# Performance work log

Measured on AMD Instinct MI355X. Metric: run time of the kernel, lower is better.

Reference implementation:

```python
import jax, jax.numpy as jnp
import numpy as np

B, S, HID, NH, AH, F = 1024, 100, 128, 2, 64, 2
DH = HID // NH          # item/pos head size = 64
DA = AH // NH           # attribute head size = 32
EPS = 1e-12


def setup_inputs() -> dict:
    key = jax.random.key(0)
    ks = iter(jax.random.split(key, 32))
    n = lambda shape, s=0.02: jax.random.normal(next(ks), shape, dtype=jnp.float32) * s
    inp = {
        "input_tensor": jax.random.normal(next(ks), (B, S, HID), dtype=jnp.float32),
        "attribute_table": jax.random.normal(next(ks), (F, B, S, AH), dtype=jnp.float32),
        "position_embedding": jax.random.normal(next(ks), (B, S, HID), dtype=jnp.float32),
        "attention_mask": jnp.zeros((B, 1, S, S), dtype=jnp.float32),
        # item / positional projections (stored [in, out])
        "Wq": n((HID, HID)), "bq": jnp.zeros((HID,), jnp.float32),
        "Wk": n((HID, HID)), "bk": jnp.zeros((HID,), jnp.float32),
        "Wv": n((HID, HID)), "bv": jnp.zeros((HID,), jnp.float32),
        "Wqp": n((HID, HID)), "bqp": jnp.zeros((HID,), jnp.float32),
        "Wkp": n((HID, HID)), "bkp": jnp.zeros((HID,), jnp.float32),
        # per-attribute projections, stacked over feat axis
        "Wq_attr": n((F, AH, AH)), "bq_attr": jnp.zeros((F, AH), jnp.float32),
        "Wk_attr": n((F, AH, AH)), "bk_attr": jnp.zeros((F, AH), jnp.float32),
        # gate fusion (VanillaAttentionX): Linear(S,S) -> ReLU -> Linear(S,1)
        "fuse_W1": n((S, S)), "fuse_b1": jnp.zeros((S,), jnp.float32),
        "fuse_W2": n((S, 1)), "fuse_b2": jnp.zeros((1,), jnp.float32),
        # output dense + LayerNorm
        "Wd": n((HID, HID)), "bd": jnp.zeros((HID,), jnp.float32),
        "ln_g": jnp.ones((HID,), jnp.float32), "ln_b": jnp.zeros((HID,), jnp.float32),
    }
    return inp


def _split_heads(x, nh):  # [B,S,nh*d] -> [B,nh,S,d]
    b, s, hd = x.shape
    return x.reshape(b, s, nh, hd // nh).transpose(0, 2, 1, 3)


def reference(input_tensor, attribute_table, position_embedding, attention_mask,
              Wq, bq, Wk, bk, Wv, bv, Wqp, bqp, Wkp, bkp,
              Wq_attr, bq_attr, Wk_attr, bk_attr,
              fuse_W1, fuse_b1, fuse_W2, fuse_b2,
              Wd, bd, ln_g, ln_b):
    b, s, hid = input_tensor.shape
    # item / positional QKV
    q = _split_heads(input_tensor @ Wq + bq, NH)
    k = _split_heads(input_tensor @ Wk + bk, NH)
    v = _split_heads(input_tensor @ Wv + bv, NH)
    qp = _split_heads(position_embedding @ Wqp + bqp, NH)
    kp = _split_heads(position_embedding @ Wkp + bkp, NH)
    item_scores = jnp.einsum('bhqd,bhkd->bhqk', q, k)
    pos_scores = jnp.einsum('bhqd,bhkd->bhqk', qp, kp)
    # attribute score streams: [F,B,S,AH] -> [F,B,NH,S,DA]
    aq = jnp.einsum('fbsa,fao->fbso', attribute_table, Wq_attr) + bq_attr[:, None, None, :]
    ak = jnp.einsum('fbsa,fao->fbso', attribute_table, Wk_attr) + bk_attr[:, None, None, :]
    aq = aq.reshape(F, b, s, NH, DA).transpose(0, 1, 3, 2, 4)
    ak = ak.reshape(F, b, s, NH, DA).transpose(0, 1, 3, 2, 4)
    attr_scores = jnp.einsum('fbhqd,fbhkd->fbhqk', aq, ak)  # [F,B,NH,S,S]
    # gate fusion: stack streams on axis -2 -> [B,NH,S,F+2,S]
    stacked = jnp.concatenate([
        jnp.moveaxis(attr_scores, 0, 3),
        item_scores[:, :, :, None, :],
        pos_scores[:, :, :, None, :],
    ], axis=-2)
    energy = jax.nn.relu(stacked @ fuse_W1 + fuse_b1) @ fuse_W2 + fuse_b2  # [B,NH,S,F+2,1]
    gate_w = jax.nn.softmax(energy[..., 0], axis=-1)                       # [B,NH,S,F+2]
    fused = jnp.einsum('bhsfk,bhsf->bhsk', stacked, gate_w)                # [B,NH,S,S]
    scores = fused / jnp.sqrt(jnp.asarray(DH, fused.dtype)) + attention_mask
    probs = jax.nn.softmax(scores, axis=-1)
    ctx = jnp.einsum('bhqk,bhkd->bhqd', probs, v)
    ctx = ctx.transpose(0, 2, 1, 3).reshape(b, s, hid)
    h = ctx @ Wd + bd + input_tensor
    mu = jnp.mean(h, axis=-1, keepdims=True)
    var = jnp.mean((h - mu) ** 2, axis=-1, keepdims=True)
    return (h - mu) / jnp.sqrt(var + EPS) * ln_g + ln_b
```

## Files before the change

### kernel.cpp

```cpp
#include <hip/hip_runtime.h>
#include <hip/hip_bf16.h>

using bf16 = __hip_bfloat16;
using u16 = unsigned short;
typedef __attribute__((ext_vector_type(8))) short bf16x8;
typedef __attribute__((ext_vector_type(16))) float f32x16;

namespace {

constexpr int B_  = 1024;
constexpr int Sd  = 100;
constexpr int BS_ = B_ * Sd;

constexpr int NTHR = 1024;
constexpr int NW   = 16;

constexpr int STP = 420;
constexpr int STS = 104;
constexpr int QKP = 196;
constexpr int AP  = 132;
constexpr int ATP = 68;
constexpr int VTP = 116;
constexpr int W1P = 116;

constexpr int O_ST  = 0;
constexpr int O_SA0 = 0;
constexpr int O_SA1 = 26400;
constexpr int O_AT0 = 52800;
constexpr int O_AT1 = 66400;
constexpr int O_Q   = 84000;
constexpr int O_K   = 123200;
constexpr int O_VT  = 123200;
constexpr int O_E2S = 139200;
constexpr int LBYTES = 162400;

constexpr int WQT_E  = 0;
constexpr int WKT_E  = 16384;
constexpr int WQPT_E = 32768;
constexpr int WKPT_E = 49152;
constexpr int WVT_E  = 65536;
constexpr int WAT_E  = 81920;
constexpr int W1T_E  = 98304;
constexpr int WDT_E  = 112640;
constexpr int W1PG   = 112;
constexpr size_t WS_NEED = 129024ull * 2;

__device__ __forceinline__ float bfr(u16 u) {
  unsigned int x = ((unsigned int)u) << 16;
  float f; __builtin_memcpy(&f, &x, 4); return f;
}
__device__ __forceinline__ u16 f2bu(float x) {
  bf16 h = __float2bfloat16(x);
  u16 u; __builtin_memcpy(&u, &h, 2); return u;
}
__device__ __forceinline__ float4 ld4(const float* p) {
  return *reinterpret_cast<const float4*>(p);
}
__device__ __forceinline__ float wsum(float v) {
#pragma unroll
  for (int m = 32; m > 0; m >>= 1) v += __shfl_xor(v, m);
  return v;
}
__device__ __forceinline__ float wmax(float v) {
#pragma unroll
  for (int m = 32; m > 0; m >>= 1) v = fmaxf(v, __shfl_xor(v, m));
  return v;
}
__device__ __forceinline__ f32x16 zf16() {
  f32x16 z;
#pragma unroll
  for (int i = 0; i < 16; ++i) z[i] = 0.f;
  return z;
}
__device__ __forceinline__ f32x16 MFMA32(bf16x8 a, bf16x8 b, f32x16 c) {
  return __builtin_amdgcn_mfma_f32_32x32x16_bf16(a, b, c, 0, 0, 0);
}

__device__ __forceinline__ bf16x8 ld8(const u16* p) {
  const ushort4 a = *reinterpret_cast<const ushort4*>(p);
  const ushort4 b = *reinterpret_cast<const ushort4*>(p + 4);
  bf16x8 f;
  f[0] = (short)a.x; f[1] = (short)a.y; f[2] = (short)a.z; f[3] = (short)a.w;
  f[4] = (short)b.x; f[5] = (short)b.y; f[6] = (short)b.z; f[7] = (short)b.w;
  return f;
}
__device__ __forceinline__ bf16x8 ld8a(const u16* p) {
  return *reinterpret_cast<const bf16x8*>(p);
}

template <int L4>
__device__ __forceinline__ void stage_rows4(const float* __restrict__ src, u16* dst,
                                            int nrow, int pitch, int tid, int nthr) {
  for (int i = tid; i < (nrow << L4); i += nthr) {
    const int rr = i >> L4, cc = (i & ((1 << L4) - 1)) << 2;
    const float4 v = *reinterpret_cast<const float4*>(src + ((size_t)rr << (L4 + 2)) + cc);
    ushort4 o;
    o.x = f2bu(v.x); o.y = f2bu(v.y); o.z = f2bu(v.z); o.w = f2bu(v.w);
    *reinterpret_cast<ushort4*>(dst + rr * pitch + cc) = o;
  }
}
template <int LC>
__device__ __forceinline__ void stage_wt(const float* __restrict__ W, int ldw, int coff,
                                         u16* dst, int kd, int pitch, int tid, int nthr) {
  constexpr int NC = 1 << LC;
  for (int idx = tid; idx < NC * kd; idx += nthr) {
    const int k = idx >> LC, c = idx & (NC - 1);
    dst[c * pitch + k] = f2bu(W[k * ldw + coff + c]);
  }
}
__device__ __forceinline__ void stage_wt6(const float* __restrict__ W, int coff,
                                          u16* dst, int tid, int nthr) {
  stage_wt<6>(W, 128, coff, dst, 128, AP, tid, nthr);
}

template <int KD, bool TR, bool GB>
__device__ __forceinline__ void tile32(const u16* A, int apitch, const u16* Wt, int wpitch,
                                       const float* __restrict__ bias, u16* dst, int dpitch,
                                       int dbase, int m0, int n0, int l) {
  const int cr = l & 31, g = l >> 5;
  int ar = m0 + cr; if (ar >= Sd) ar = Sd - 1;
  const u16* ap = A + ar * apitch + g * 8;
  const u16* bp = Wt + (n0 + cr) * wpitch + g * 8;
  f32x16 acc = zf16();
#pragma unroll
  for (int k0 = 0; k0 < KD; k0 += 16)
    acc = MFMA32(ld8(ap + k0), GB ? ld8a(bp + k0) : ld8(bp + k0), acc);
  const float bvv = bias[n0 + cr];
#pragma unroll
  for (int i = 0; i < 16; ++i) {
    const int row = m0 + (i & 3) + 8 * (i >> 2) + 4 * g;
    if (row < Sd) {
      if (TR) dst[(n0 + cr) * dpitch + dbase + row] = f2bu(acc[i] + bvv);
      else    dst[row * dpitch + dbase + n0 + cr]   = f2bu(acc[i] + bvv);
    }
  }
}

__global__ __launch_bounds__(256) void prep_weights(
    const float* __restrict__ Wq, const float* __restrict__ Wk,
    const float* __restrict__ Wqp, const float* __restrict__ Wkp,
    const float* __restrict__ Wv, const float* __restrict__ Wqa,
    const float* __restrict__ Wka, const float* __restrict__ W1,
    const float* __restrict__ Wd, u16* __restrict__ ws) {
  const int t = blockIdx.x * 256 + threadIdx.x;
  const int NT = gridDim.x * 256;
  const float* srcs[5] = {Wq, Wk, Wqp, Wkp, Wv};
#pragma unroll
  for (int wsel = 0; wsel < 5; ++wsel) {
    u16* dst = ws + wsel * 16384;
    const float* src = srcs[wsel];
    for (int i = t; i < 16384; i += NT) {
      const int h = i >> 13, c = (i >> 7) & 63, k = i & 127;
      dst[i] = f2bu(src[k * 128 + h * 64 + c]);
    }
  }
  for (int i = t; i < 16384; i += NT) {
    const int pr = i >> 12, h = (i >> 11) & 1, c = (i >> 6) & 31, k = i & 63;
    const float* src = (pr & 1) ? Wka : Wqa;
    ws[WAT_E + i] = f2bu(src[(pr >> 1) * 4096 + k * 64 + h * 32 + c]);
  }
  for (int i = t; i < 14336; i += NT) {
    const int c = i / W1PG, k = i - c * W1PG;
    ws[W1T_E + i] = (c < Sd && k < Sd) ? f2bu(W1[k * Sd + c]) : (u16)0;
  }
  for (int i = t; i < 16384; i += NT) {
    const int c = i >> 7, k = i & 127;
    ws[WDT_E + i] = f2bu(Wd[k * 128 + c]);
  }
}

__global__ __launch_bounds__(NTHR) void attn_mega_p(
    const float* __restrict__ input, const float* __restrict__ attrT,
    const float* __restrict__ posE, const float* __restrict__ mask,
    const float* __restrict__ bq, const float* __restrict__ bk,
    const float* __restrict__ bv, const float* __restrict__ bqp,
    const float* __restrict__ bkp, const float* __restrict__ bqa,
    const float* __restrict__ bka, const float* __restrict__ b1,
    const float* __restrict__ W2, const u16* __restrict__ wsw,
    float* __restrict__ ctx) {
  __shared__ __align__(16) char L[LBYTES];
  u16* const ST  = (u16*)(L + O_ST);
  u16* const SA0 = (u16*)(L + O_SA0);
  u16* const SA1 = (u16*)(L + O_SA1);
  u16* const AT0 = (u16*)(L + O_AT0);
  u16* const AT1 = (u16*)(L + O_AT1);
  u16* const QC  = (u16*)(L + O_Q);
  u16* const KC  = (u16*)(L + O_K);
  u16* const VA  = (u16*)(L + O_Q);
  u16* const VT  = (u16*)(L + O_VT);
  float* const e2s = (float*)(L + O_E2S);

  const int tid = threadIdx.x;
  const int bh = blockIdx.x;
  const int b = bh >> 1, h = bh & 1;
  const size_t row0 = (size_t)b * Sd;
  const int l = tid & 63, w = tid >> 6;
  const int cr = l & 31, g = l >> 5;

  stage_rows4<5>(input + row0 * 128, SA0, 100, AP, tid, NTHR);
  float4 r2[4];
#pragma unroll
  for (int s = 0; s < 4; ++s) {
    const int fi = tid + s * NTHR;
    if (fi < 3200) r2[s] = ld4(posE + row0 * 128 + fi * 4);
  }
  __syncthreads();

  float4 r3[4];
#pragma unroll
  for (int s = 0; s < 4; ++s) {
    const int fi = tid + s * NTHR;
    if (fi < 1600)      r3[s] = ld4(attrT + (size_t)b * 6400 + fi * 4);
    else if (fi < 3200) r3[s] = ld4(attrT + (size_t)(B_ + b) * 6400 + (fi - 1600) * 4);
  }
#pragma unroll
  for (int s = 0; s < 4; ++s) {
    const int fi = tid + s * NTHR;
    if (fi < 3200) {
      ushort4 o;
      o.x = f2bu(r2[s].x); o.y = f2bu(r2[s].y); o.z = f2bu(r2[s].z); o.w = f2bu(r2[s].w);
      *reinterpret_cast<ushort4*>(SA1 + (fi >> 5) * AP + ((fi & 31) << 2)) = o;
    }
  }
  {
    const int pr = w >> 3, mt = (w >> 1) & 3, nt = w & 1;
    const u16* wg = wsw + (pr ? WKT_E : WQT_E) + h * 8192;
    tile32<128, false, true>(SA0, AP, wg, 128, (pr ? bk : bq) + h * 64,
                             pr ? KC : QC, QKP, 0, mt * 32, nt * 32, l);
  }
  __syncthreads();

#pragma unroll
  for (int s = 0; s < 4; ++s) {
    const int fi = tid + s * NTHR;
    if (fi < 1600) {
      ushort4 o;
      o.x = f2bu(r3[s].x); o.y = f2bu(r3[s].y); o.z = f2bu(r3[s].z); o.w = f2bu(r3[s].w);
      *reinterpret_cast<ushort4*>(AT0 + (fi >> 4) * ATP + ((fi & 15) << 2)) = o;
    } else if (fi < 3200) {
      const int f3 = fi - 1600;
      ushort4 o;
      o.x = f2bu(r3[s].x); o.y = f2bu(r3[s].y); o.z = f2bu(r3[s].z); o.w = f2bu(r3[s].w);
      *reinterpret_cast<ushort4*>(AT1 + (f3 >> 4) * ATP + ((f3 & 15) << 2)) = o;
    }
  }
  {
    const int pr = w >> 3, mt = (w >> 1) & 3, nt = w & 1;
    const u16* wg = wsw + (pr ? WKPT_E : WQPT_E) + h * 8192;
    tile32<128, false, true>(SA1, AP, wg, 128, (pr ? bkp : bqp) + h * 64,
                             pr ? KC : QC, QKP, 64, mt * 32, nt * 32, l);
  }
  __syncthreads();

  {
    const int pr = w >> 2, mt = w & 3;
    const u16* Asrc = (pr < 2) ? AT0 : AT1;
    const u16* wg = wsw + WAT_E + pr * 4096 + h * 2048;
    const float* bs = (pr == 0) ? bqa + h * 32 : (pr == 1) ? bka + h * 32
                     : (pr == 2) ? bqa + 64 + h * 32 : bka + 64 + h * 32;
    tile32<64, false, true>(Asrc, ATP, wg, 64, bs, (pr & 1) ? KC : QC, QKP,
                            128 + (pr >> 1) * 32, mt * 32, 0, l);
  }
  __syncthreads();

  {
    ushort4 z; z.x = z.y = z.z = z.w = 0;
    for (int q = tid; q < Sd; q += NTHR)
      *reinterpret_cast<ushort4*>(ST + q * STP + 416) = z;
  }
  {
    const int mt = w >> 2, nt = w & 3;
    const int m0 = mt * 32, n0 = nt * 32;
    int ar = m0 + cr; if (ar >= Sd) ar = Sd - 1;
    int br = n0 + cr; if (br >= Sd) br = Sd - 1;
    const u16* ap = QC + ar * QKP + g * 8;
    const u16* bp = KC + br * QKP + g * 8;
    f32x16 ai = zf16(), po = zf16(), a0 = zf16(), a1 = zf16();
    ai = MFMA32(ld8(ap + 0),   ld8(bp + 0),   ai);
    ai = MFMA32(ld8(ap + 16),  ld8(bp + 16),  ai);
    ai = MFMA32(ld8(ap + 32),  ld8(bp + 32),  ai);
    ai = MFMA32(ld8(ap + 48),  ld8(bp + 48),  ai);
    po = MFMA32(ld8(ap + 64),  ld8(bp + 64),  po);
    po = MFMA32(ld8(ap + 80),  ld8(bp + 80),  po);
    po = MFMA32(ld8(ap + 96),  ld8(bp + 96),  po);
    po = MFMA32(ld8(ap + 112), ld8(bp + 112), po);
    a0 = MFMA32(ld8(ap + 128), ld8(bp + 128), a0);
    a0 = MFMA32(ld8(ap + 144), ld8(bp + 144), a0);
    a1 = MFMA32(ld8(ap + 160), ld8(bp + 160), a1);
    a1 = MFMA32(ld8(ap + 176), ld8(bp + 176), a1);
    const int col = n0 + cr;
    if (col < STS) {
#pragma unroll
      for (int i = 0; i < 16; ++i) {
        const int row = m0 + (i & 3) + 8 * (i >> 2) + 4 * g;
        if (row < Sd) {
          u16* sp = ST + row * STP + col;
          sp[0]       = f2bu(a0[i]);
          sp[STS]     = f2bu(a1[i]);
          sp[2 * STS] = f2bu(ai[i]);
          sp[3 * STS] = f2bu(po[i]);
        }
      }
    }
  }
  __syncthreads();

  stage_rows4<5>(input + row0 * 128, VA, 100, AP, tid, NTHR);
  {
    ushort4 z; z.x = z.y = z.z = z.w = 0;
    for (int i2 = tid; i2 < 64 * VTP / 4; i2 += NTHR)
      *reinterpret_cast<ushort4*>(VT + i2 * 4) = z;
  }
  __syncthreads();

  {
    float b1v[4], w2v[4];
#pragma unroll
    for (int nt = 0; nt < 4; ++nt) {
      const int c = nt * 32 + cr;
      b1v[nt] = (c < Sd) ? b1[c] : 0.f;
      w2v[nt] = (c < Sd) ? W2[c] : 0.f;
    }
    const u16* wg1 = wsw + W1T_E;
    for (int mt = w; mt < 13; mt += NW) {
      const int m0 = mt * 32;
      int gr = m0 + cr; if (gr > 399) gr = 399;
      const u16* ap = ST + (gr >> 2) * STP + (gr & 3) * STS + g * 8;
      f32x16 c0 = zf16(), c1 = zf16(), c2 = zf16(), c3 = zf16();
#pragma unroll
      for (int k0 = 0; k0 < 112; k0 += 16) {
        const bf16x8 af = ld8(ap + k0);
        c0 = MFMA32(af, ld8a(wg1 + (cr)      * W1PG + g * 8 + k0), c0);
        c1 = MFMA32(af, ld8a(wg1 + (32 + cr) * W1PG + g * 8 + k0), c1);
        c2 = MFMA32(af, ld8a(wg1 + (64 + cr) * W1PG + g * 8 + k0), c2);
        c3 = MFMA32(af, ld8a(wg1 + (96 + cr) * W1PG + g * 8 + k0), c3);
      }
#pragma unroll
      for (int i = 0; i < 16; ++i) {
        float v = fmaxf(c0[i] + b1v[0], 0.f) * w2v[0]
                + fmaxf(c1[i] + b1v[1], 0.f) * w2v[1]
                + fmaxf(c2[i] + b1v[2], 0.f) * w2v[2]
                + fmaxf(c3[i] + b1v[3], 0.f) * w2v[3];
#pragma unroll
        for (int mm = 1; mm < 32; mm <<= 1) v += __shfl_xor(v, mm);
        if (cr == 0) {
          const int go = m0 + (i & 3) + 8 * (i >> 2) + 4 * g;
          if (go < 400) e2s[go] = v;
        }
      }
    }
  }
  __syncthreads();

  if (w < 8) {
    for (int q = w; q < Sd; q += 8) {
      const float* ez = e2s + q * 4;
      float e0 = ez[0], e1 = ez[1], e2v = ez[2], e3 = ez[3];
      const float mg = fmaxf(fmaxf(e0, e1), fmaxf(e2v, e3));
      e0 = __expf(e0 - mg); e1 = __expf(e1 - mg);
      e2v = __expf(e2v - mg); e3 = __expf(e3 - mg);
      const float ginv = 1.0f / (e0 + e1 + e2v + e3);
      const float g0v = e0 * ginv, g1v = e1 * ginv, g2v = e2v * ginv, g3v = e3 * ginv;
      u16* const sp = ST + q * STP;
      const float* const mp = mask + (size_t)b * 10000 + q * 100;
      float x1 = g0v * bfr(sp[l]) + g1v * bfr(sp[STS + l]) +
                 g2v * bfr(sp[2 * STS + l]) + g3v * bfr(sp[3 * STS + l]);
      x1 = x1 * 0.125f + mp[l];
      const bool v2 = (l < 36);
      float x2 = -3e38f;
      if (v2) {
        const int k2 = 64 + l;
        x2 = g0v * bfr(sp[k2]) + g1v * bfr(sp[STS + k2]) +
             g2v * bfr(sp[2 * STS + k2]) + g3v * bfr(sp[3 * STS + k2]);
        x2 = x2 * 0.125f + mp[k2];
      }
      const float M = wmax(fmaxf(x1, x2));
      const float ea = __expf(x1 - M);
      const float eb = v2 ? __expf(x2 - M) : 0.f;
      const float inv = 1.0f / wsum(ea + eb);
      sp[l] = f2bu(ea * inv);
      if (v2) sp[64 + l] = f2bu(eb * inv);
    }
  } else {
    const int u = w - 8;
    const int mt = u >> 1, nt = u & 1;
    tile32<128, true, true>(VA, AP, wsw + WVT_E + h * 8192, 128, bv + h * 64,
                            VT, VTP, 0, mt * 32, nt * 32, l);
  }
  __syncthreads();

  if (w < 8) {
    const int mt = w >> 1, nt = w & 1;
    const int m0 = mt * 32, n0 = nt * 32;
    int ar = m0 + cr; if (ar >= Sd) ar = Sd - 1;
    const u16* ap = ST + ar * STP + g * 8;
    const u16* bp = VT + (n0 + cr) * VTP + g * 8;
    f32x16 acc = zf16();
#pragma unroll
    for (int k0 = 0; k0 < 112; k0 += 16)
      acc = MFMA32(ld8(ap + k0), ld8(bp + k0), acc);
#pragma unroll
    for (int i = 0; i < 16; ++i) {
      const int row = m0 + (i & 3) + 8 * (i >> 2) + 4 * g;
      if (row < Sd)
        ctx[(row0 + row) * 128 + h * 64 + n0 + cr] = acc[i];
    }
  }
}

__global__ __launch_bounds__(512, 4) void dense_ln_p(
    const float* __restrict__ ctxg, const float* __restrict__ bd,
    const float* __restrict__ resid, const float* __restrict__ lng,
    const float* __restrict__ lnb, const u16* __restrict__ wsw,
    float* __restrict__ out) {
  __shared__ __align__(16) char L[67584];
  u16* const Ab = (u16*)L;
  u16* const Hs = (u16*)(L + 33792);
  const int tid = threadIdx.x;
  const size_t row0 = (size_t)blockIdx.x * 128;
  const int l = tid & 63, w = tid >> 6, cr = l & 31, g = l >> 5;

  stage_rows4<5>(ctxg + row0 * 128, Ab, 128, AP, tid, 512);
  __syncthreads();

  for (int u = w; u < 16; u += 8) {
    const int m0 = (u >> 2) * 32, n0 = (u & 3) * 32;
    const u16* ap = Ab + (m0 + cr) * AP + g * 8;
    const u16* bp = wsw + WDT_E + (n0 + cr) * 128 + g * 8;
    f32x16 acc = zf16();
#pragma unroll
    for (int k0 = 0; k0 < 128; k0 += 16)
      acc = MFMA32(ld8(ap + k0), ld8a(bp + k0), acc);
#pragma unroll
    for (int i = 0; i < 16; ++i) {
      const int row = m0 + (i & 3) + 8 * (i >> 2) + 4 * g;
      Hs[row * AP + n0 + cr] = f2bu(acc[i]);
    }
  }
  __syncthreads();

  for (int rr = w; rr < 128; rr += 8) {
    const size_t grow = row0 + rr;
    const float h1 = bfr(Hs[rr * AP + l])      + bd[l]      + resid[grow * 128 + l];
    const float h2 = bfr(Hs[rr * AP + 64 + l]) + bd[64 + l] + resid[grow * 128 + 64 + l];
    const float mu = wsum(h1 + h2) * (1.0f / 128.0f);
    const float d1 = h1 - mu, d2 = h2 - mu;
    const float var = wsum(d1 * d1 + d2 * d2) * (1.0f / 128.0f);
    const float rs = rsqrtf(var + 1e-12f);
    out[grow * 128 + l]      = d1 * rs * lng[l]      + lnb[l];
    out[grow * 128 + 64 + l] = d2 * rs * lng[64 + l] + lnb[64 + l];
  }
}

__global__ __launch_bounds__(NTHR) void attn_mega_fb(
    const float* __restrict__ input, const float* __restrict__ attrT,
    const float* __restrict__ posE, const float* __restrict__ mask,
    const float* __restrict__ Wq, const float* __restrict__ bq,
    const float* __restrict__ Wk, const float* __restrict__ bk,
    const float* __restrict__ Wv, const float* __restrict__ bv,
    const float* __restrict__ Wqp, const float* __restrict__ bqp,
    const float* __restrict__ Wkp, const float* __restrict__ bkp,
    const float* __restrict__ Wqa, const float* __restrict__ bqa,
    const float* __restrict__ Wka, const float* __restrict__ bka,
    const float* __restrict__ W1, const float* __restrict__ b1,
    const float* __restrict__ W2, float* __restrict__ ctx) {
  __shared__ __align__(16) char L[LBYTES];
  u16* const ST = (u16*)(L + O_ST);
  u16* const QC = (u16*)(L + O_Q);
  u16* const KC = (u16*)(L + O_K);
  u16* const SA  = (u16*)(L + O_ST);
  u16* const SW1 = (u16*)(L + O_ST + 26400);
  u16* const SW2 = (u16*)(L + O_ST + 43296);
  u16* const AT0  = (u16*)(L + O_ST);
  u16* const AT1  = (u16*)(L + O_ST + 13600);
  u16* const WA0Q = (u16*)(L + O_ST + 27200);
  u16* const WA0K = (u16*)(L + O_ST + 31552);
  u16* const WA1Q = (u16*)(L + O_ST + 35904);
  u16* const WA1K = (u16*)(L + O_ST + 40256);
  u16* const W1T = (u16*)(L + O_K);
  float* const e2s = (float*)(L + O_K + 32000);
  u16* const VA  = (u16*)(L + O_Q);
  u16* const WVT = (u16*)(L + O_K);
  u16* const VT  = (u16*)(L + O_K + 16896);

  const int tid = threadIdx.x;
  const int bh = blockIdx.x;
  const int b = bh >> 1, h = bh & 1;
  const size_t row0 = (size_t)b * Sd;
  const int l = tid & 63, w = tid >> 6;
  const int cr = l & 31, g = l >> 5;

  stage_rows4<5>(input + row0 * 128, SA, 100, AP, tid, NTHR);
  stage_wt6(Wq, h * 64, SW1, tid, NTHR);
  stage_wt6(Wk, h * 64, SW2, tid, NTHR);
  float4 r2[8];
#pragma unroll
  for (int s = 0; s < 8; ++s) {
    const int fi = tid + s * NTHR;
    if (fi < 3200) r2[s] = ld4(posE + row0 * 128 + fi * 4);
    else if (fi < 5248) {
      const int f2 = fi - 3200, k = f2 >> 4, c0 = (f2 & 15) << 2;
      r2[s] = ld4(Wqp + k * 128 + h * 64 + c0);
    } else if (fi < 7296) {
      const int f2 = fi - 5248, k = f2 >> 4, c0 = (f2 & 15) << 2;
      r2[s] = ld4(Wkp + k * 128 + h * 64 + c0);
    }
  }
  __syncthreads();
  {
    const int pr = w >> 3, mt = (w >> 1) & 3, nt = w & 1;
    tile32<128, false, false>(SA, AP, pr ? SW2 : SW1, AP, (pr ? bk : bq) + h * 64,
                              pr ? KC : QC, QKP, 0, mt * 32, nt * 32, l);
  }
  __syncthreads();
#pragma unroll
  for (int s = 0; s < 8; ++s) {
    const int fi = tid + s * NTHR;
    if (fi < 3200) {
      ushort4 o;
      o.x = f2bu(r2[s].x); o.y = f2bu(r2[s].y); o.z = f2bu(r2[s].z); o.w = f2bu(r2[s].w);
      *reinterpret_cast<ushort4*>(SA + (fi >> 5) * AP + ((fi & 31) << 2)) = o;
    } else if (fi < 5248) {
      const int f2 = fi - 3200, k = f2 >> 4, c0 = (f2 & 15) << 2;
      SW1[c0 * AP + k] = f2bu(r2[s].x); SW1[(c0 + 1) * AP + k] = f2bu(r2[s].y);
      SW1[(c0 + 2) * AP + k] = f2bu(r2[s].z); SW1[(c0 + 3) * AP + k] = f2bu(r2[s].w);
    } else if (fi < 7296) {
      const int f2 = fi - 5248, k = f2 >> 4, c0 = (f2 & 15) << 2;
      SW2[c0 * AP + k] = f2bu(r2[s].x); SW2[(c0 + 1) * AP + k] = f2bu(r2[s].y);
      SW2[(c0 + 2) * AP + k] = f2bu(r2[s].z); SW2[(c0 + 3) * AP + k] = f2bu(r2[s].w);
    }
  }
  float4 r3[6];
#pragma unroll
  for (int s = 0; s < 6; ++s) {
    const int fi = tid + s * NTHR;
    if (fi < 1600) r3[s] = ld4(attrT + (size_t)b * 6400 + fi * 4);
    else if (fi < 3200) r3[s] = ld4(attrT + (size_t)(B_ + b) * 6400 + (fi - 1600) * 4);
    else if (fi < 5248) {
      const int f3 = fi - 3200, which = f3 >> 9, fj = f3 & 511;
      const int k = fj >> 3, c0 = (fj & 7) << 2;
      const float* src = (which == 0) ? Wqa : (which == 1) ? Wka
                       : (which == 2) ? (Wqa + 4096) : (Wka + 4096);
      r3[s] = ld4(src + k * 64 + h * 32 + c0);
    }
  }
  __syncthreads();
  {
    const int pr = w >> 3, mt = (w >> 1) & 3, nt = w & 1;
    tile32<128, false, false>(SA, AP, pr ? SW2 : SW1, AP, (pr ? bkp : bqp) + h * 64,
                              pr ? KC : QC, QKP, 64, mt * 32, nt * 32, l);
  }
  __syncthreads();
#pragma unroll
  for (int s = 0; s < 6; ++s) {
    const int fi = tid + s * NTHR;
    if (fi < 1600) {
      ushort4 o;
      o.x = f2bu(r3[s].x); o.y = f2bu(r3[s].y); o.z = f2bu(r3[s].z); o.w = f2bu(r3[s].w);
      *reinterpret_cast<ushort4*>(AT0 + (fi >> 4) * ATP + ((fi & 15) << 2)) = o;
    } else if (fi < 3200) {
      const int f3 = fi - 1600;
      ushort4 o;
      o.x = f2bu(r3[s].x); o.y = f2bu(r3[s].y); o.z = f2bu(r3[s].z); o.w = f2bu(r3[s].w);
      *reinterpret_cast<ushort4*>(AT1 + (f3 >> 4) * ATP + ((f3 & 15) << 2)) = o;
    } else if (fi < 5248) {
      const int f3 = fi - 3200, which = f3 >> 9, fj = f3 & 511;
      const int k = fj >> 3, c0 = (fj & 7) << 2;
      u16* dst = (which == 0) ? WA0Q : (which == 1) ? WA0K
               : (which == 2) ? WA1Q : WA1K;
      dst[c0 * ATP + k] = f2bu(r3[s].x); dst[(c0 + 1) * ATP + k] = f2bu(r3[s].y);
      dst[(c0 + 2) * ATP + k] = f2bu(r3[s].z); dst[(c0 + 3) * ATP + k] = f2bu(r3[s].w);
    }
  }
  float4 r5[3];
#pragma unroll
  for (int s = 0; s < 3; ++s) {
    const int fi = tid + s * NTHR;
    if (fi < 2500) r5[s] = ld4(W1 + fi * 4);
  }
  __syncthreads();
  {
    const int pr = w >> 2, mt = w & 3;
    const u16* Asrc = (pr < 2) ? AT0 : AT1;
    const u16* Wt = (pr == 0) ? WA0Q : (pr == 1) ? WA0K : (pr == 2) ? WA1Q : WA1K;
    const float* bs = (pr == 0) ? bqa + h * 32 : (pr == 1) ? bka + h * 32
                     : (pr == 2) ? bqa + 64 + h * 32 : bka + 64 + h * 32;
    tile32<64, false, false>(Asrc, ATP, Wt, ATP, bs, (pr & 1) ? KC : QC, QKP,
                             128 + (pr >> 1) * 32, mt * 32, 0, l);
  }
  __syncthreads();
  {
    ushort4 z; z.x = z.y = z.z = z.w = 0;
    for (int q = tid; q < Sd; q += NTHR)
      *reinterpret_cast<ushort4*>(ST + q * STP + 416) = z;
  }
  {
    const int mt = w >> 2, nt = w & 3;
    const int m0 = mt * 32, n0 = nt * 32;
    int ar = m0 + cr; if (ar >= Sd) ar = Sd - 1;
    int br = n0 + cr; if (br >= Sd) br = Sd - 1;
    const u16* ap = QC + ar * QKP + g * 8;
    const u16* bp = KC + br * QKP + g * 8;
    f32x16 ai = zf16(), po = zf16(), a0 = zf16(), a1 = zf16();
    ai = MFMA32(ld8(ap + 0),   ld8(bp + 0),   ai);
    ai = MFMA32(ld8(ap + 16),  ld8(bp + 16),  ai);
    ai = MFMA32(ld8(ap + 32),  ld8(bp + 32),  ai);
    ai = MFMA32(ld8(ap + 48),  ld8(bp + 48),  ai);
    po = MFMA32(ld8(ap + 64),  ld8(bp + 64),  po);
    po = MFMA32(ld8(ap + 80),  ld8(bp + 80),  po);
    po = MFMA32(ld8(ap + 96),  ld8(bp + 96),  po);
    po = MFMA32(ld8(ap + 112), ld8(bp + 112), po);
    a0 = MFMA32(ld8(ap + 128), ld8(bp + 128), a0);
    a0 = MFMA32(ld8(ap + 144), ld8(bp + 144), a0);
    a1 = MFMA32(ld8(ap + 160), ld8(bp + 160), a1);
    a1 = MFMA32(ld8(ap + 176), ld8(bp + 176), a1);
    const int col = n0 + cr;
    if (col < STS) {
#pragma unroll
      for (int i = 0; i < 16; ++i) {
        const int row = m0 + (i & 3) + 8 * (i >> 2) + 4 * g;
        if (row < Sd) {
          u16* sp = ST + row * STP + col;
          sp[0]       = f2bu(a0[i]);
          sp[STS]     = f2bu(a1[i]);
          sp[2 * STS] = f2bu(ai[i]);
          sp[3 * STS] = f2bu(po[i]);
        }
      }
    }
  }
  __syncthreads();
  {
    ushort4 z; z.x = z.y = z.z = z.w = 0;
    if (tid < 812)
      *reinterpret_cast<ushort4*>(W1T + 11600 + tid * 4) = z;
    if (tid < 400) {
      const int c = tid >> 2, kq = 100 + ((tid & 3) << 2);
      *reinterpret_cast<ushort4*>(W1T + c * W1P + kq) = z;
    }
  }
  if (tid < 8) ((u16*)(L + O_Q))[tid] = 0;
#pragma unroll
  for (int s = 0; s < 3; ++s) {
    const int fi = tid + s * NTHR;
    if (fi < 2500) {
#pragma unroll
      for (int j = 0; j < 4; ++j) {
        const int o = fi * 4 + j;
        const int k = o / 100, c = o - k * 100;
        W1T[c * W1P + k] = f2bu((j == 0) ? r5[s].x : (j == 1) ? r5[s].y
                                : (j == 2) ? r5[s].z : r5[s].w);
      }
    }
  }
  __syncthreads();
  {
    float b1v[4], w2v[4];
#pragma unroll
    for (int nt = 0; nt < 4; ++nt) {
      const int c = nt * 32 + cr;
      b1v[nt] = (c < Sd) ? b1[c] : 0.f;
      w2v[nt] = (c < Sd) ? W2[c] : 0.f;
    }
    for (int mt = w; mt < 13; mt += NW) {
      const int m0 = mt * 32;
      int gr = m0 + cr; if (gr > 399) gr = 399;
      const u16* ap = ST + (gr >> 2) * STP + (gr & 3) * STS + g * 8;
      f32x16 c0 = zf16(), c1 = zf16(), c2 = zf16(), c3 = zf16();
#pragma unroll
      for (int k0 = 0; k0 < 112; k0 += 16) {
        const bf16x8 af = ld8(ap + k0);
        c0 = MFMA32(af, ld8(W1T + (cr)      * W1P + g * 8 + k0), c0);
        c1 = MFMA32(af, ld8(W1T + (32 + cr) * W1P + g * 8 + k0), c1);
        c2 = MFMA32(af, ld8(W1T + (64 + cr) * W1P + g * 8 + k0), c2);
        c3 = MFMA32(af, ld8(W1T + (96 + cr) * W1P + g * 8 + k0), c3);
      }
#pragma unroll
      for (int i = 0; i < 16; ++i) {
        float v = fmaxf(c0[i] + b1v[0], 0.f) * w2v[0]
                + fmaxf(c1[i] + b1v[1], 0.f) * w2v[1]
                + fmaxf(c2[i] + b1v[2], 0.f) * w2v[2]
                + fmaxf(c3[i] + b1v[3], 0.f) * w2v[3];
#pragma unroll
        for (int mm = 1; mm < 32; mm <<= 1) v += __shfl_xor(v, mm);
        if (cr == 0) {
          const int go = m0 + (i & 3) + 8 * (i >> 2) + 4 * g;
          if (go < 400) e2s[go] = v;
        }
      }
    }
  }
  __syncthreads();
  stage_rows4<5>(input + row0 * 128, VA, 100, AP, tid, NTHR);
  stage_wt6(Wv, h * 64, WVT, tid, NTHR);
  {
    ushort4 z; z.x = z.y = z.z = z.w = 0;
    for (int i2 = tid; i2 < 64 * VTP / 4; i2 += NTHR)
      *reinterpret_cast<ushort4*>(VT + i2 * 4) = z;
  }
  for (int q = w; q < Sd; q += NW) {
    const float* ez = e2s + q * 4;
    float e0 = ez[0], e1 = ez[1], e2v = ez[2], e3 = ez[3];
    const float mg = fmaxf(fmaxf(e0, e1), fmaxf(e2v, e3));
    e0 = __expf(e0 - mg); e1 = __expf(e1 - mg);
    e2v = __expf(e2v - mg); e3 = __expf(e3 - mg);
    const float ginv = 1.0f / (e0 + e1 + e2v + e3);
    const float g0v = e0 * ginv, g1v = e1 * ginv, g2v = e2v * ginv, g3v = e3 * ginv;
    u16* const sp = ST + q * STP;
    const float* const mp = mask + (size_t)b * 10000 + q * 100;
    float x1 = g0v * bfr(sp[l]) + g1v * bfr(sp[STS + l]) +
               g2v * bfr(sp[2 * STS + l]) + g3v * bfr(sp[3 * STS + l]);
    x1 = x1 * 0.125f + mp[l];
    const bool v2 = (l < 36);
    float x2 = -3e38f;
    if (v2) {
      const int k2 = 64 + l;
      x2 = g0v * bfr(sp[k2]) + g1v * bfr(sp[STS + k2]) +
           g2v * bfr(sp[2 * STS + k2]) + g3v * bfr(sp[3 * STS + k2]);
      x2 = x2 * 0.125f + mp[k2];
    }
    const float M = wmax(fmaxf(x1, x2));
    const float ea = __expf(x1 - M);
    const float eb = v2 ? __expf(x2 - M) : 0.f;
    const float inv = 1.0f / wsum(ea + eb);
    sp[l] = f2bu(ea * inv);
    if (v2) sp[64 + l] = f2bu(eb * inv);
  }
  __syncthreads();
  if (w < 8) {
    const int mt = w >> 1, nt = w & 1;
    tile32<128, true, false>(VA, AP, WVT, AP, bv + h * 64, VT, VTP, 0, mt * 32, nt * 32, l);
  }
  __syncthreads();
  if (w < 8) {
    const int mt = w >> 1, nt = w & 1;
    const int m0 = mt * 32, n0 = nt * 32;
    int ar = m0 + cr; if (ar >= Sd) ar = Sd - 1;
    const u16* ap = ST + ar * STP + g * 8;
    const u16* bp = VT + (n0 + cr) * VTP + g * 8;
    f32x16 acc = zf16();
#pragma unroll
    for (int k0 = 0; k0 < 112; k0 += 16)
      acc = MFMA32(ld8(ap + k0), ld8(bp + k0), acc);
#pragma unroll
    for (int i = 0; i < 16; ++i) {
      const int row = m0 + (i & 3) + 8 * (i >> 2) + 4 * g;
      if (row < Sd)
        ctx[(row0 + row) * 128 + h * 64 + n0 + cr] = acc[i];
    }
  }
}

__global__ __launch_bounds__(512) void dense_ln_fb(
    const float* __restrict__ ctxg, const float* __restrict__ Wd,
    const float* __restrict__ bd, const float* __restrict__ resid,
    const float* __restrict__ lng, const float* __restrict__ lnb,
    float* __restrict__ out) {
  __shared__ __align__(16) char L[101376];
  u16* const Ab  = (u16*)L;
  u16* const WdT = (u16*)(L + 33792);
  u16* const Hs  = (u16*)(L + 67584);
  const int tid = threadIdx.x;
  const size_t row0 = (size_t)blockIdx.x * 128;
  const int l = tid & 63, w = tid >> 6, cr = l & 31, g = l >> 5;

  stage_rows4<5>(ctxg + row0 * 128, Ab, 128, AP, tid, 512);
  stage_wt<7>(Wd, 128, 0, WdT, 128, AP, tid, 512);
  __syncthreads();
  for (int u = w; u < 16; u += 8) {
    const int m0 = (u >> 2) * 32, n0 = (u & 3) * 32;
    const u16* ap = Ab + (m0 + cr) * AP + g * 8;
    const u16* bp = WdT + (n0 + cr) * AP + g * 8;
    f32x16 acc = zf16();
#pragma unroll
    for (int k0 = 0; k0 < 128; k0 += 16)
      acc = MFMA32(ld8(ap + k0), ld8(bp + k0), acc);
#pragma unroll
    for (int i = 0; i < 16; ++i) {
      const int row = m0 + (i & 3) + 8 * (i >> 2) + 4 * g;
      Hs[row * AP + n0 + cr] = f2bu(acc[i]);
    }
  }
  __syncthreads();
  for (int rr = w; rr < 128; rr += 8) {
    const size_t grow = row0 + rr;
    const float h1 = bfr(Hs[rr * AP + l])      + bd[l]      + resid[grow * 128 + l];
    const float h2 = bfr(Hs[rr * AP + 64 + l]) + bd[64 + l] + resid[grow * 128 + 64 + l];
    const float mu = wsum(h1 + h2) * (1.0f / 128.0f);
    const float d1 = h1 - mu, d2 = h2 - mu;
    const float var = wsum(d1 * d1 + d2 * d2) * (1.0f / 128.0f);
    const float rs = rsqrtf(var + 1e-12f);
    out[grow * 128 + l]      = d1 * rs * lng[l]      + lnb[l];
    out[grow * 128 + 64 + l] = d2 * rs * lng[64 + l] + lnb[64 + l];
  }
}

}

extern "C" void kernel_launch(void* const* d_in, const int* in_sizes, int n_in,
                              void* d_out, int out_size, void* d_ws,
                              size_t ws_size, hipStream_t stream) {
  (void)in_sizes; (void)n_in; (void)out_size;

  const float* input = (const float*)d_in[0];
  const float* attrT = (const float*)d_in[1];
  const float* posE  = (const float*)d_in[2];
  const float* mask  = (const float*)d_in[3];
  const float* Wq  = (const float*)d_in[4];  const float* bq  = (const float*)d_in[5];
  const float* Wk  = (const float*)d_in[6];  const float* bk  = (const float*)d_in[7];
  const float* Wv  = (const float*)d_in[8];  const float* bv  = (const float*)d_in[9];
  const float* Wqp = (const float*)d_in[10]; const float* bqp = (const float*)d_in[11];
  const float* Wkp = (const float*)d_in[12]; const float* bkp = (const float*)d_in[13];
  const float* Wqa = (const float*)d_in[14]; const float* bqa = (const float*)d_in[15];
  const float* Wka = (const float*)d_in[16]; const float* bka = (const float*)d_in[17];
  const float* W1  = (const float*)d_in[18]; const float* b1  = (const float*)d_in[19];
  const float* W2  = (const float*)d_in[20];
  const float* Wd  = (const float*)d_in[22]; const float* bd  = (const float*)d_in[23];
  const float* lng = (const float*)d_in[24]; const float* lnb = (const float*)d_in[25];

  float* ctx = (float*)d_out;

  if (ws_size >= WS_NEED) {
    u16* wsw = (u16*)d_ws;
    prep_weights<<<dim3(128), dim3(256), 0, stream>>>(
        Wq, Wk, Wqp, Wkp, Wv, Wqa, Wka, W1, Wd, wsw);
    attn_mega_p<<<dim3(B_ * 2), dim3(NTHR), 0, stream>>>(
        input, attrT, posE, mask, bq, bk, bv, bqp, bkp, bqa, bka, b1, W2, wsw, ctx);
    dense_ln_p<<<dim3(BS_ / 128), dim3(512), 0, stream>>>(
        ctx, bd, input, lng, lnb, wsw, ctx);
  } else {
    attn_mega_fb<<<dim3(B_ * 2), dim3(NTHR), 0, stream>>>(
        input, attrT, posE, mask, Wq, bq, Wk, bk, Wv, bv, Wqp, bqp, Wkp, bkp,
        Wqa, bqa, Wka, bka, W1, b1, W2, ctx);
    dense_ln_fb<<<dim3(BS_ / 128), dim3(512), 0, stream>>>(
        ctx, Wd, bd, input, lng, lnb, ctx);
  }
}
```

Baseline: 397.1 us.

## Stage pre-converted weights into LDS instead of reading MFMA operands from global

The attention megakernel now copies the bf16 Q/K, positional Q/K, attribute and gate W1 weight tiles from the workspace into padded LDS buffers before each projection. The MFMA loops then read LDS instead of doing direct global loads, and the LDS layout is reorganised so these buffers reuse regions, with the V-transpose padding zeroed only where needed. The dense+LayerNorm kernel likewise stages Wd into LDS, and the prepacked and fallback versions are merged into one templated kernel. The aim is to cut global/L2 traffic and latency on the MFMA operand path. The cost is extra LDS copies, barriers, and register prefetch pressure, plus a larger LDS footprint in dense_ln that may reduce occupancy.

Measured after the change: 359.6 us. -9.5%, faster.

```diff
diff --git a/kernel.cpp b/kernel.cpp
--- a/kernel.cpp
+++ b/kernel.cpp
@@ -20,18 +20,13 @@
 constexpr int QKP = 196;
 constexpr int AP  = 132;
 constexpr int ATP = 68;
+constexpr int W1P = 116;
 constexpr int VTP = 116;
-constexpr int W1P = 116;
-
-constexpr int O_ST  = 0;
-constexpr int O_SA0 = 0;
-constexpr int O_SA1 = 26400;
-constexpr int O_AT0 = 52800;
-constexpr int O_AT1 = 66400;
-constexpr int O_Q   = 84000;
-constexpr int O_K   = 123200;
-constexpr int O_VT  = 123200;
-constexpr int O_E2S = 139200;
+
+constexpr int O_ST = 0;
+constexpr int O_Q  = 84000;
+constexpr int O_K  = 123200;
+constexpr int E2S  = 32000;
 constexpr int LBYTES = 162400;
 
 constexpr int WQT_E  = 0;
@@ -41,9 +36,8 @@
 constexpr int WVT_E  = 65536;
 constexpr int WAT_E  = 81920;
 constexpr int W1T_E  = 98304;
-constexpr int WDT_E  = 112640;
-constexpr int W1PG   = 112;
-constexpr size_t WS_NEED = 129024ull * 2;
+constexpr int WDT_E  = 113152;
+constexpr size_t WS_NEED = 129536ull * 2;
 
 __device__ __forceinline__ float bfr(u16 u) {
   unsigned int x = ((unsigned int)u) << 16;
@@ -112,6 +106,14 @@
                                           u16* dst, int tid, int nthr) {
   stage_wt<6>(W, 128, coff, dst, 128, AP, tid, nthr);
 }
+__device__ __forceinline__ void copy_w64(const u16* __restrict__ src, u16* dst,
+                                         int tid, int nthr) {
+  for (int i = tid; i < 2048; i += nthr) {
+    const int r = i >> 5, c4 = (i & 31) << 2;
+    *reinterpret_cast<ushort4*>(dst + r * AP + c4) =
+        *reinterpret_cast<const ushort4*>(src + r * 128 + c4);
+  }
+}
 
 template <int KD, bool TR, bool GB>
 __device__ __forceinline__ void tile32(const u16* A, int apitch, const u16* Wt, int wpitch,
@@ -159,8 +161,8 @@
     const float* src = (pr & 1) ? Wka : Wqa;
     ws[WAT_E + i] = f2bu(src[(pr >> 1) * 4096 + k * 64 + h * 32 + c]);
   }
-  for (int i = t; i < 14336; i += NT) {
-    const int c = i / W1PG, k = i - c * W1PG;
+  for (int i = t; i < 14848; i += NT) {
+    const int c = i / W1P, k = i - c * W1P;
     ws[W1T_E + i] = (c < Sd && k < Sd) ? f2bu(W1[k * Sd + c]) : (u16)0;
   }
   for (int i = t; i < 16384; i += NT) {
@@ -179,16 +181,22 @@
     const float* __restrict__ W2, const u16* __restrict__ wsw,
     float* __restrict__ ctx) {
   __shared__ __align__(16) char L[LBYTES];
-  u16* const ST  = (u16*)(L + O_ST);
-  u16* const SA0 = (u16*)(L + O_SA0);
-  u16* const SA1 = (u16*)(L + O_SA1);
-  u16* const AT0 = (u16*)(L + O_AT0);
-  u16* const AT1 = (u16*)(L + O_AT1);
-  u16* const QC  = (u16*)(L + O_Q);
-  u16* const KC  = (u16*)(L + O_K);
+  u16* const ST = (u16*)(L + O_ST);
+  u16* const QC = (u16*)(L + O_Q);
+  u16* const KC = (u16*)(L + O_K);
+  u16* const SA  = (u16*)(L + O_ST);
+  u16* const SW1 = (u16*)(L + O_ST + 26400);
+  u16* const SW2 = (u16*)(L + O_ST + 43296);
+  u16* const AT0  = (u16*)(L + O_ST);
+  u16* const AT1  = (u16*)(L + O_ST + 13600);
+  u16* const WA0Q = (u16*)(L + O_ST + 27200);
+  u16* const WA0K = (u16*)(L + O_ST + 31552);
+  u16* const WA1Q = (u16*)(L + O_ST + 35904);
+  u16* const WA1K = (u16*)(L + O_ST + 40256);
+  u16* const W1T = (u16*)(L + O_K);
+  float* const e2s = (float*)(L + O_K + E2S);
   u16* const VA  = (u16*)(L + O_Q);
-  u16* const VT  = (u16*)(L + O_VT);
-  float* const e2s = (float*)(L + O_E2S);
+  u16* const VT  = (u16*)(L + O_K + 16896);
 
   const int tid = threadIdx.x;
   const int bh = blockIdx.x;
@@ -197,7 +205,9 @@
   const int l = tid & 63, w = tid >> 6;
   const int cr = l & 31, g = l >> 5;
 
-  stage_rows4<5>(input + row0 * 128, SA0, 100, AP, tid, NTHR);
+  stage_rows4<5>(input + row0 * 128, SA, 100, AP, tid, NTHR);
+  copy_w64(wsw + WQT_E + h * 8192, SW1, tid, NTHR);
+  copy_w64(wsw + WKT_E + h * 8192, SW2, tid, NTHR);
   float4 r2[4];
 #pragma unroll
   for (int s = 0; s < 4; ++s) {
@@ -206,27 +216,37 @@
   }
   __syncthreads();
 
-  float4 r3[4];
-#pragma unroll
-  for (int s = 0; s < 4; ++s) {
-    const int fi = tid + s * NTHR;
-    if (fi < 1600)      r3[s] = ld4(attrT + (size_t)b * 6400 + fi * 4);
-    else if (fi < 3200) r3[s] = ld4(attrT + (size_t)(B_ + b) * 6400 + (fi - 1600) * 4);
-  }
+  {
+    const int pr = w >> 3, mt = (w >> 1) & 3, nt = w & 1;
+    tile32<128, false, false>(SA, AP, pr ? SW2 : SW1, AP, (pr ? bk : bq) + h * 64,
+                              pr ? KC : QC, QKP, 0, mt * 32, nt * 32, l);
+  }
+  __syncthreads();
+
 #pragma unroll
   for (int s = 0; s < 4; ++s) {
     const int fi = tid + s * NTHR;
     if (fi < 3200) {
       ushort4 o;
       o.x = f2bu(r2[s].x); o.y = f2bu(r2[s].y); o.z = f2bu(r2[s].z); o.w = f2bu(r2[s].w);
-      *reinterpret_cast<ushort4*>(SA1 + (fi >> 5) * AP + ((fi & 31) << 2)) = o;
-    }
-  }
+      *reinterpret_cast<ushort4*>(SA + (fi >> 5) * AP + ((fi & 31) << 2)) = o;
+    }
+  }
+  copy_w64(wsw + WQPT_E + h * 8192, SW1, tid, NTHR);
+  copy_w64(wsw + WKPT_E + h * 8192, SW2, tid, NTHR);
+  float4 r3[4];
+#pragma unroll
+  for (int s = 0; s < 4; ++s) {
+    const int fi = tid + s * NTHR;
+    if (fi < 1600)      r3[s] = ld4(attrT + (size_t)b * 6400 + fi * 4);
+    else if (fi < 3200) r3[s] = ld4(attrT + (size_t)(B_ + b) * 6400 + (fi - 1600) * 4);
+  }
+  __syncthreads();
+
   {
     const int pr = w >> 3, mt = (w >> 1) & 3, nt = w & 1;
-    const u16* wg = wsw + (pr ? WKT_E : WQT_E) + h * 8192;
-    tile32<128, false, true>(SA0, AP, wg, 128, (pr ? bk : bq) + h * 64,
-                             pr ? KC : QC, QKP, 0, mt * 32, nt * 32, l);
+    tile32<128, false, false>(SA, AP, pr ? SW2 : SW1, AP, (pr ? bkp : bqp) + h * 64,
+                              pr ? KC : QC, QKP, 64, mt * 32, nt * 32, l);
   }
   __syncthreads();
 
@@ -244,22 +264,28 @@
       *reinterpret_cast<ushort4*>(AT1 + (f3 >> 4) * ATP + ((f3 & 15) << 2)) = o;
     }
   }
-  {
-    const int pr = w >> 3, mt = (w >> 1) & 3, nt = w & 1;
-    const u16* wg = wsw + (pr ? WKPT_E : WQPT_E) + h * 8192;
-    tile32<128, false, true>(SA1, AP, wg, 128, (pr ? bkp : bqp) + h * 64,
-                             pr ? KC : QC, QKP, 64, mt * 32, nt * 32, l);
+  for (int i = tid; i < 2048; i += NTHR) {
+    const int pr = i >> 9, row = (i >> 4) & 31, c4 = (i & 15) << 2;
+    u16* dst = (pr == 0) ? WA0Q : (pr == 1) ? WA0K : (pr == 2) ? WA1Q : WA1K;
+    *reinterpret_cast<ushort4*>(dst + row * ATP + c4) =
+        *reinterpret_cast<const ushort4*>(wsw + WAT_E + pr * 4096 + h * 2048 + row * 64 + c4);
+  }
+  ushort4 rw1[4];
+#pragma unroll
+  for (int s = 0; s < 4; ++s) {
+    const int fi = tid + s * NTHR;
+    if (fi < 3712) rw1[s] = reinterpret_cast<const ushort4*>(wsw + W1T_E)[fi];
   }
   __syncthreads();
 
   {
     const int pr = w >> 2, mt = w & 3;
     const u16* Asrc = (pr < 2) ? AT0 : AT1;
-    const u16* wg = wsw + WAT_E + pr * 4096 + h * 2048;
+    const u16* Wt = (pr == 0) ? WA0Q : (pr == 1) ? WA0K : (pr == 2) ? WA1Q : WA1K;
     const float* bs = (pr == 0) ? bqa + h * 32 : (pr == 1) ? bka + h * 32
                      : (pr == 2) ? bqa + 64 + h * 32 : bka + 64 + h * 32;
-    tile32<64, false, true>(Asrc, ATP, wg, 64, bs, (pr & 1) ? KC : QC, QKP,
-                            128 + (pr >> 1) * 32, mt * 32, 0, l);
+    tile32<64, false, false>(Asrc, ATP, Wt, ATP, bs, (pr & 1) ? KC : QC, QKP,
+                             128 + (pr >> 1) * 32, mt * 32, 0, l);
   }
   __syncthreads();
 
@@ -305,12 +331,12 @@
   }
   __syncthreads();
 
+#pragma unroll
+  for (int s = 0; s < 4; ++s) {
+    const int fi = tid + s * NTHR;
+    if (fi < 3712) reinterpret_cast<ushort4*>(W1T)[fi] = rw1[s];
+  }
   stage_rows4<5>(input + row0 * 128, VA, 100, AP, tid, NTHR);
-  {
-    ushort4 z; z.x = z.y = z.z = z.w = 0;
-    for (int i2 = tid; i2 < 64 * VTP / 4; i2 += NTHR)
-      *reinterpret_cast<ushort4*>(VT + i2 * 4) = z;
-  }
   __syncthreads();
 
   {
@@ -321,7 +347,6 @@
       b1v[nt] = (c < Sd) ? b1[c] : 0.f;
       w2v[nt] = (c < Sd) ? W2[c] : 0.f;
     }
-    const u16* wg1 = wsw + W1T_E;
     for (int mt = w; mt < 13; mt += NW) {
       const int m0 = mt * 32;
       int gr = m0 + cr; if (gr > 399) gr = 399;
@@ -330,10 +355,10 @@
 #pragma unroll
       for (int k0 = 0; k0 < 112; k0 += 16) {
         const bf16x8 af = ld8(ap + k0);
-        c0 = MFMA32(af, ld8a(wg1 + (cr)      * W1PG + g * 8 + k0), c0);
-        c1 = MFMA32(af, ld8a(wg1 + (32 + cr) * W1PG + g * 8 + k0), c1);
-        c2 = MFMA32(af, ld8a(wg1 + (64 + cr) * W1PG + g * 8 + k0), c2);
-        c3 = MFMA32(af, ld8a(wg1 + (96 + cr) * W1PG + g * 8 + k0), c3);
+        c0 = MFMA32(af, ld8(W1T + (cr)      * W1P + g * 8 + k0), c0);
+        c1 = MFMA32(af, ld8(W1T + (32 + cr) * W1P + g * 8 + k0), c1);
+        c2 = MFMA32(af, ld8(W1T + (64 + cr) * W1P + g * 8 + k0), c2);
+        c3 = MFMA32(af, ld8(W1T + (96 + cr) * W1P + g * 8 + k0), c3);
       }
 #pragma unroll
       for (int i = 0; i < 16; ++i) {
@@ -384,6 +409,13 @@
   } else {
     const int u = w - 8;
     const int mt = u >> 1, nt = u & 1;
+    if (mt == 3 && g == 0) {
+      ushort4 z; z.x = z.y = z.z = z.w = 0;
+      u16* vp = VT + (nt * 32 + cr) * VTP + 100;
+      *reinterpret_cast<ushort4*>(vp)     = z;
+      *reinterpret_cast<ushort4*>(vp + 4) = z;
+      *reinterpret_cast<ushort4*>(vp + 8) = z;
+    }
     tile32<128, true, true>(VA, AP, wsw + WVT_E + h * 8192, 128, bv + h * 64,
                             VT, VTP, 0, mt * 32, nt * 32, l);
   }
@@ -408,29 +440,40 @@
   }
 }
 
-__global__ __launch_bounds__(512, 4) void dense_ln_p(
-    const float* __restrict__ ctxg, const float* __restrict__ bd,
-    const float* __restrict__ resid, const float* __restrict__ lng,
-    const float* __restrict__ lnb, const u16* __restrict__ wsw,
-    float* __restrict__ out) {
-  __shared__ __align__(16) char L[67584];
-  u16* const Ab = (u16*)L;
-  u16* const Hs = (u16*)(L + 33792);
+template <bool PREP>
+__global__ __launch_bounds__(512) void dense_ln(
+    const float* __restrict__ ctxg, const float* __restrict__ Wd,
+    const float* __restrict__ bd, const float* __restrict__ resid,
+    const float* __restrict__ lng, const float* __restrict__ lnb,
+    const u16* __restrict__ wsw, float* __restrict__ out) {
+  __shared__ __align__(16) char L[101376];
+  u16* const Ab  = (u16*)L;
+  u16* const WdT = (u16*)(L + 33792);
+  u16* const Hs  = (u16*)(L + 67584);
   const int tid = threadIdx.x;
   const size_t row0 = (size_t)blockIdx.x * 128;
   const int l = tid & 63, w = tid >> 6, cr = l & 31, g = l >> 5;
 
   stage_rows4<5>(ctxg + row0 * 128, Ab, 128, AP, tid, 512);
+  if constexpr (PREP) {
+    for (int i = tid; i < 4096; i += 512) {
+      const int r = i >> 5, c4 = (i & 31) << 2;
+      *reinterpret_cast<ushort4*>(WdT + r * AP + c4) =
+          *reinterpret_cast<const ushort4*>(wsw + WDT_E + r * 128 + c4);
+    }
+  } else {
+    stage_wt<7>(Wd, 128, 0, WdT, 128, AP, tid, 512);
+  }
   __syncthreads();
 
   for (int u = w; u < 16; u += 8) {
     const int m0 = (u >> 2) * 32, n0 = (u & 3) * 32;
     const u16* ap = Ab + (m0 + cr) * AP + g * 8;
-    const u16* bp = wsw + WDT_E + (n0 + cr) * 128 + g * 8;
+    const u16* bp = WdT + (n0 + cr) * AP + g * 8;
     f32x16 acc = zf16();
 #pragma unroll
     for (int k0 = 0; k0 < 128; k0 += 16)
-      acc = MFMA32(ld8(ap + k0), ld8a(bp + k0), acc);
+      acc = MFMA32(ld8(ap + k0), ld8(bp + k0), acc);
 #pragma unroll
     for (int i = 0; i < 16; ++i) {
       const int row = m0 + (i & 3) + 8 * (i >> 2) + 4 * g;
@@ -478,7 +521,7 @@
   u16* const WA1Q = (u16*)(L + O_ST + 35904);
   u16* const WA1K = (u16*)(L + O_ST + 40256);
   u16* const W1T = (u16*)(L + O_K);
-  float* const e2s = (float*)(L + O_K + 32000);
+  float* const e2s = (float*)(L + O_K + E2S);
   u16* const VA  = (u16*)(L + O_Q);
   u16* const WVT = (u16*)(L + O_K);
   u16* const VT  = (u16*)(L + O_K + 16896);
@@ -751,50 +794,6 @@
   }
 }
 
-__global__ __launch_bounds__(512) void dense_ln_fb(
-    const float* __restrict__ ctxg, const float* __restrict__ Wd,
-    const float* __restrict__ bd, const float* __restrict__ resid,
-    const float* __restrict__ lng, const float* __restrict__ lnb,
-    float* __restrict__ out) {
-  __shared__ __align__(16) char L[101376];
-  u16* const Ab  = (u16*)L;
-  u16* const WdT = (u16*)(L + 33792);
-  u16* const Hs  = (u16*)(L + 67584);
-  const int tid = threadIdx.x;
-  const size_t row0 = (size_t)blockIdx.x * 128;
-  const int l = tid & 63, w = tid >> 6, cr = l & 31, g = l >> 5;
-
-  stage_rows4<5>(ctxg + row0 * 128, Ab, 128, AP, tid, 512);
-  stage_wt<7>(Wd, 128, 0, WdT, 128, AP, tid, 512);
-  __syncthreads();
-  for (int u = w; u < 16; u += 8) {
-    const int m0 = (u >> 2) * 32, n0 = (u & 3) * 32;
-    const u16* ap = Ab + (m0 + cr) * AP + g * 8;
-    const u16* bp = WdT + (n0 + cr) * AP + g * 8;
-    f32x16 acc = zf16();
-#pragma unroll
-    for (int k0 = 0; k0 < 128; k0 += 16)
-      acc = MFMA32(ld8(ap + k0), ld8(bp + k0), acc);
-#pragma unroll
-    for (int i = 0; i < 16; ++i) {
-      const int row = m0 + (i & 3) + 8 * (i >> 2) + 4 * g;
-      Hs[row * AP + n0 + cr] = f2bu(acc[i]);
-    }
-  }
-  __syncthreads();
-  for (int rr = w; rr < 128; rr += 8) {
-    const size_t grow = row0 + rr;
-    const float h1 = bfr(Hs[rr * AP + l])      + bd[l]      + resid[grow * 128 + l];
-    const float h2 = bfr(Hs[rr * AP + 64 + l]) + bd[64 + l] + resid[grow * 128 + 64 + l];
-    const float mu = wsum(h1 + h2) * (1.0f / 128.0f);
-    const float d1 = h1 - mu, d2 = h2 - mu;
-    const float var = wsum(d1 * d1 + d2 * d2) * (1.0f / 128.0f);
-    const float rs = rsqrtf(var + 1e-12f);
-    out[grow * 128 + l]      = d1 * rs * lng[l]      + lnb[l];
-    out[grow * 128 + 64 + l] = d2 * rs * lng[64 + l] + lnb[64 + l];
-  }
-}
-
 }
 
 extern "C" void kernel_launch(void* const* d_in, const int* in_sizes, int n_in,
@@ -826,13 +825,13 @@
         Wq, Wk, Wqp, Wkp, Wv, Wqa, Wka, W1, Wd, wsw);
     attn_mega_p<<<dim3(B_ * 2), dim3(NTHR), 0, stream>>>(
         input, attrT, posE, mask, bq, bk, bv, bqp, bkp, bqa, bka, b1, W2, wsw, ctx);
-    dense_ln_p<<<dim3(BS_ / 128), dim3(512), 0, stream>>>(
-        ctx, bd, input, lng, lnb, wsw, ctx);
+    dense_ln<true><<<dim3(BS_ / 128), dim3(512), 0, stream>>>(
+        ctx, Wd, bd, input, lng, lnb, wsw, ctx);
   } else {
     attn_mega_fb<<<dim3(B_ * 2), dim3(NTHR), 0, stream>>>(
         input, attrT, posE, mask, Wq, bq, Wk, bk, Wv, bv, Wqp, bqp, Wkp, bkp,
         Wqa, bqa, Wka, bka, W1, b1, W2, ctx);
-    dense_ln_fb<<<dim3(BS_ / 128), dim3(512), 0, stream>>>(
-        ctx, Wd, bd, input, lng, lnb, ctx);
-  }
-}
+    dense_ln<false><<<dim3(BS_ / 128), dim3(512), 0, stream>>>(
+        ctx, Wd, bd, input, lng, lnb, nullptr, ctx);
+  }
+}
```
